# Optimization experiments

Measured on AMD Instinct MI355X. Metric: run time of the kernel, lower is better.

## Reference

```python
import jax, jax.numpy as jnp
import numpy as np

EMB = 1024
HEADS = 16
DEPTH = EMB // HEADS
B, S = 8, 1024


def setup_inputs() -> dict:
    key = jax.random.key(0)
    ks = jax.random.split(key, 12)
    sc = 0.02
    return {
        "q": jax.random.normal(ks[0], (B, S, EMB), jnp.float32),
        "k": jax.random.normal(ks[1], (B, S, EMB), jnp.float32),
        "v": jax.random.normal(ks[2], (B, S, EMB), jnp.float32),
        # per-head Dense weights stacked: [H, EMB, DEPTH], biases [H, DEPTH]
        "Wq": jax.random.normal(ks[3], (HEADS, EMB, DEPTH), jnp.float32) * sc,
        "bq": jnp.zeros((HEADS, DEPTH), jnp.float32),
        "Wk": jax.random.normal(ks[4], (HEADS, EMB, DEPTH), jnp.float32) * sc,
        "bk": jnp.zeros((HEADS, DEPTH), jnp.float32),
        "Wv": jax.random.normal(ks[5], (HEADS, EMB, DEPTH), jnp.float32) * sc,
        "bv": jnp.zeros((HEADS, DEPTH), jnp.float32),
        # output Dense: [EMB, EMB], bias [EMB]
        "Wo": jax.random.normal(ks[6], (EMB, EMB), jnp.float32) * sc,
        "bo": jnp.zeros((EMB,), jnp.float32),
    }


def reference(q, k, v, Wq, bq, Wk, bk, Wv, bv, Wo, bo):
    # Per-head Dense projections, batched over heads via einsum.
    # qh: [B, H, S, DEPTH]
    qh = jnp.einsum("bsd,hde->bhse", q, Wq) + bq[None, :, None, :]
    kh = jnp.einsum("bsd,hde->bhse", k, Wk) + bk[None, :, None, :]
    vh = jnp.einsum("bsd,hde->bhse", v, Wv) + bv[None, :, None, :]
    # Scaled dot-product attention per head: logits [B, H, Sq, Sk]
    scale = 1.0 / jnp.sqrt(jnp.asarray(DEPTH, jnp.float32))
    logits = jnp.einsum("bhqe,bhke->bhqk", qh, kh) * scale
    attn = jax.nn.softmax(logits, axis=-1)
    ctx = jnp.einsum("bhqk,bhke->bhqe", attn, vh)  # [B, H, S, DEPTH]
    # concat heads along last axis (head order preserved)
    ctx = jnp.transpose(ctx, (0, 2, 1, 3)).reshape(B, S, EMB)
    return ctx @ Wo + bo
```

## Files before the change

### kernel.cpp

```cpp
#include <hip/hip_runtime.h>
#include <hip/hip_bf16.h>
#include <stdint.h>

typedef __bf16 bf16;
typedef __attribute__((ext_vector_type(8))) __bf16 bf16x8;
typedef __attribute__((ext_vector_type(4))) float f32x4;

#define GLD(g, l) __builtin_amdgcn_global_load_lds( \
    (const __attribute__((address_space(1))) void*)(g), \
    (__attribute__((address_space(3))) void*)(l), 16, 0, 0)

__device__ __forceinline__ f32x4 mfma16(bf16x8 a, bf16x8 b, f32x4 c) {
  return __builtin_amdgcn_mfma_f32_16x16x32_bf16(a, b, c, 0, 0, 0);
}

__global__ __launch_bounds__(256) void cast_k(const float* __restrict__ s,
                                              bf16* __restrict__ d)
{
  const size_t i = ((size_t)blockIdx.x * 256 + threadIdx.x) * 8;
  float4 a = *(const float4*)(s + i);
  float4 b = *(const float4*)(s + i + 4);
  bf16x8 p;
  p[0] = (bf16)a.x; p[1] = (bf16)a.y; p[2] = (bf16)a.z; p[3] = (bf16)a.w;
  p[4] = (bf16)b.x; p[5] = (bf16)b.y; p[6] = (bf16)b.z; p[7] = (bf16)b.w;
  *(bf16x8*)(d + i) = p;
}

template <typename ST>
__global__ void transpose_k(const ST* __restrict__ src, bf16* __restrict__ dst,
                            int sld, int dld, int sdiv, int sA, int sB, int dA, int dB)
{
  __shared__ bf16 t[32][33];
  const int z = blockIdx.z;
  const ST* s = src + (size_t)(z / sdiv) * sA + (size_t)(z % sdiv) * sB;
  bf16* d = dst + (size_t)(z / sdiv) * dA + (size_t)(z % sdiv) * dB;
  const int c0 = blockIdx.x * 32, r0 = blockIdx.y * 32;
  const int tx = threadIdx.x, ty = threadIdx.y;
#pragma unroll
  for (int i = 0; i < 32; i += 8)
    t[ty + i][tx] = (bf16)(float)s[(r0 + ty + i) * sld + c0 + tx];
  __syncthreads();
#pragma unroll
  for (int i = 0; i < 32; i += 8)
    d[(c0 + ty + i) * dld + r0 + tx] = t[tx][ty + i];
}

__global__ __launch_bounds__(256) void gemm_bt(
    const bf16* __restrict__ A, const bf16* __restrict__ Bt,
    const float* __restrict__ bias, bf16* __restrict__ C,
    int M, int N, int K, float cmul)
{
  __shared__ bf16 sA[128 * 32];
  __shared__ bf16 sB[128 * 32];
  const int tid = threadIdx.x;
  const int wave = tid >> 6, lane = tid & 63;
  const int lr = lane & 15, kq = (lane >> 4) * 8;
  const int m0 = blockIdx.y * 128, n0 = blockIdx.x * 128;
  const int wr = (wave >> 1) * 64, wc = (wave & 1) * 64;

  f32x4 acc[4][4];
#pragma unroll
  for (int i = 0; i < 4; i++)
#pragma unroll
    for (int j = 0; j < 4; j++)
#pragma unroll
      for (int e = 0; e < 4; e++) acc[i][j][e] = 0.f;

  const int sRow = tid >> 2;
  const int sKo = (tid & 3) * 8;
  const bf16* aPtr = A + (size_t)(m0 + sRow) * K + sKo;
  const bf16* bPtr = Bt + (size_t)(n0 + sRow) * K + sKo;
  bf16* sAd = sA + tid * 8;
  bf16* sBd = sB + tid * 8;

  for (int k0 = 0; k0 < K; k0 += 32) {
    GLD(aPtr + k0,           sAd);
    GLD(aPtr + 64 * K + k0,  sAd + 2048);
    GLD(bPtr + k0,           sBd);
    GLD(bPtr + 64 * K + k0,  sBd + 2048);
    __syncthreads();
    bf16x8 af[4], bfr[4];
#pragma unroll
    for (int i = 0; i < 4; i++)
      af[i] = *(const bf16x8*)(sA + (wr + i * 16 + lr) * 32 + kq);
#pragma unroll
    for (int i = 0; i < 4; i++)
      bfr[i] = *(const bf16x8*)(sB + (wc + i * 16 + lr) * 32 + kq);
#pragma unroll
    for (int im = 0; im < 4; im++)
#pragma unroll
      for (int in = 0; in < 4; in++)
        acc[im][in] = mfma16(af[im], bfr[in], acc[im][in]);
    __syncthreads();
  }

  const int qd = (lane >> 4) * 4;
  float bv[4];
#pragma unroll
  for (int in = 0; in < 4; in++) bv[in] = bias[n0 + wc + in * 16 + lr];
#pragma unroll
  for (int im = 0; im < 4; im++) {
    const int row = m0 + wr + im * 16 + qd;
#pragma unroll
    for (int in = 0; in < 4; in++) {
      const int col = n0 + wc + in * 16 + lr;
#pragma unroll
      for (int i = 0; i < 4; i++)
        C[(size_t)(row + i) * N + col] = (bf16)((acc[im][in][i] + bv[in]) * cmul);
    }
  }
}

__global__ __launch_bounds__(256) void gemm_a16_c32(
    const bf16* __restrict__ A, const bf16* __restrict__ Bt,
    const float* __restrict__ bias, float* __restrict__ C,
    int M, int N, int K)
{
  __shared__ bf16 sA[128 * 32];
  __shared__ bf16 sB[128 * 32];
  const int tid = threadIdx.x;
  const int wave = tid >> 6, lane = tid & 63;
  const int lr = lane & 15, kq = (lane >> 4) * 8;
  const int m0 = blockIdx.y * 128, n0 = blockIdx.x * 128;
  const int wr = (wave >> 1) * 64, wc = (wave & 1) * 64;

  f32x4 acc[4][4];
#pragma unroll
  for (int i = 0; i < 4; i++)
#pragma unroll
    for (int j = 0; j < 4; j++)
#pragma unroll
      for (int e = 0; e < 4; e++) acc[i][j][e] = 0.f;

  const int sRow = tid >> 2;
  const int sKo = (tid & 3) * 8;
  const bf16* aPtr = A + (size_t)(m0 + sRow) * K + sKo;
  const bf16* bPtr = Bt + (size_t)(n0 + sRow) * K + sKo;
  bf16* sAd = sA + tid * 8;
  bf16* sBd = sB + tid * 8;

  for (int k0 = 0; k0 < K; k0 += 32) {
    GLD(aPtr + k0,           sAd);
    GLD(aPtr + 64 * K + k0,  sAd + 2048);
    GLD(bPtr + k0,           sBd);
    GLD(bPtr + 64 * K + k0,  sBd + 2048);
    __syncthreads();
    bf16x8 af[4], bfr[4];
#pragma unroll
    for (int i = 0; i < 4; i++)
      af[i] = *(const bf16x8*)(sA + (wr + i * 16 + lr) * 32 + kq);
#pragma unroll
    for (int i = 0; i < 4; i++)
      bfr[i] = *(const bf16x8*)(sB + (wc + i * 16 + lr) * 32 + kq);
#pragma unroll
    for (int im = 0; im < 4; im++)
#pragma unroll
      for (int in = 0; in < 4; in++)
        acc[im][in] = mfma16(af[im], bfr[in], acc[im][in]);
    __syncthreads();
  }

  const int qd = (lane >> 4) * 4;
  float bv[4];
#pragma unroll
  for (int in = 0; in < 4; in++) bv[in] = bias[n0 + wc + in * 16 + lr];
#pragma unroll
  for (int im = 0; im < 4; im++) {
    const int row = m0 + wr + im * 16 + qd;
#pragma unroll
    for (int in = 0; in < 4; in++) {
      const int col = n0 + wc + in * 16 + lr;
#pragma unroll
      for (int i = 0; i < 4; i++)
        C[(size_t)(row + i) * N + col] = acc[im][in][i] + bv[in];
    }
  }
}

__global__ __launch_bounds__(256) void attn_k(
    const bf16* __restrict__ Q, const bf16* __restrict__ Kh,
    const bf16* __restrict__ Vt, bf16* __restrict__ O)
{
  __shared__ bf16 sK[64 * 72];
  __shared__ bf16 sV[64 * 72];
  __shared__ bf16 sP[128 * 72];
  const int h = blockIdx.x, b = blockIdx.y, q0 = blockIdx.z * 128;
  const int tid = threadIdx.x, wave = tid >> 6, lane = tid & 63;
  const int lr = lane & 15, quad = lane >> 4, kq = quad * 8;
  const int wq = wave * 32;

  const bf16* Qb = Q + (size_t)(b * 1024 + q0) * 1024 + h * 64;
  const bf16* Kb = Kh + (size_t)(b * 1024) * 1024 + h * 64;
  const bf16* Vb = Vt + (size_t)(b * 16 + h) * 65536;

  bf16x8 qf[2][2];
#pragma unroll
  for (int rg = 0; rg < 2; rg++)
#pragma unroll
    for (int ks = 0; ks < 2; ks++)
      qf[rg][ks] = *(const bf16x8*)(Qb + (wq + rg * 16 + lr) * 1024 + ks * 32 + kq);

  f32x4 o[2][4];
  float rsum[2][4];
#pragma unroll
  for (int rg = 0; rg < 2; rg++) {
#pragma unroll
    for (int et = 0; et < 4; et++)
#pragma unroll
      for (int e = 0; e < 4; e++) o[rg][et][e] = 0.f;
#pragma unroll
    for (int i = 0; i < 4; i++) rsum[rg][i] = 0.f;
  }

  const int r = tid >> 3;
  const int c = (tid & 7) * 8;

  for (int kv0 = 0; kv0 < 1024; kv0 += 64) {
    bf16x8 k1 = *(const bf16x8*)(Kb + (size_t)(kv0 + r) * 1024 + c);
    bf16x8 k2 = *(const bf16x8*)(Kb + (size_t)(kv0 + 32 + r) * 1024 + c);
    bf16x8 v1 = *(const bf16x8*)(Vb + (size_t)r * 1024 + kv0 + c);
    bf16x8 v2 = *(const bf16x8*)(Vb + (size_t)(32 + r) * 1024 + kv0 + c);
    __syncthreads();
    *(bf16x8*)(sK + r * 72 + c) = k1;
    *(bf16x8*)(sK + (32 + r) * 72 + c) = k2;
    *(bf16x8*)(sV + r * 72 + c) = v1;
    *(bf16x8*)(sV + (32 + r) * 72 + c) = v2;
    __syncthreads();

    f32x4 sc[2][4];
#pragma unroll
    for (int nt = 0; nt < 4; nt++) {
      bf16x8 kf0 = *(const bf16x8*)(sK + (nt * 16 + lr) * 72 + kq);
      bf16x8 kf1 = *(const bf16x8*)(sK + (nt * 16 + lr) * 72 + 32 + kq);
#pragma unroll
      for (int rg = 0; rg < 2; rg++) {
        f32x4 z;
#pragma unroll
        for (int e = 0; e < 4; e++) z[e] = 0.f;
        z = mfma16(qf[rg][0], kf0, z);
        z = mfma16(qf[rg][1], kf1, z);
        sc[rg][nt] = z;
      }
    }

#pragma unroll
    for (int rg = 0; rg < 2; rg++)
#pragma unroll
      for (int i = 0; i < 4; i++) {
        float p0 = exp2f(sc[rg][0][i]);
        float p1 = exp2f(sc[rg][1][i]);
        float p2 = exp2f(sc[rg][2][i]);
        float p3 = exp2f(sc[rg][3][i]);
        rsum[rg][i] += (p0 + p1) + (p2 + p3);
        const int prow = (wq + rg * 16 + quad * 4 + i) * 72;
        sP[prow + 0 * 16 + lr] = (bf16)p0;
        sP[prow + 1 * 16 + lr] = (bf16)p1;
        sP[prow + 2 * 16 + lr] = (bf16)p2;
        sP[prow + 3 * 16 + lr] = (bf16)p3;
      }
    __syncthreads();

#pragma unroll
    for (int et = 0; et < 4; et++) {
      bf16x8 vf0 = *(const bf16x8*)(sV + (et * 16 + lr) * 72 + kq);
      bf16x8 vf1 = *(const bf16x8*)(sV + (et * 16 + lr) * 72 + 32 + kq);
#pragma unroll
      for (int rg = 0; rg < 2; rg++) {
        bf16x8 pa = *(const bf16x8*)(sP + (wq + rg * 16 + lr) * 72 + kq);
        bf16x8 pb = *(const bf16x8*)(sP + (wq + rg * 16 + lr) * 72 + 32 + kq);
        o[rg][et] = mfma16(pa, vf0, o[rg][et]);
        o[rg][et] = mfma16(pb, vf1, o[rg][et]);
      }
    }
  }

#pragma unroll
  for (int rg = 0; rg < 2; rg++)
#pragma unroll
    for (int i = 0; i < 4; i++) {
      float rs = rsum[rg][i];
#pragma unroll
      for (int off = 1; off < 16; off <<= 1)
        rs += __shfl_xor(rs, off, 64);
      rsum[rg][i] = 1.f / rs;
    }

  bf16* Ob = O + (size_t)(b * 1024 + q0) * 1024 + h * 64;
#pragma unroll
  for (int rg = 0; rg < 2; rg++)
#pragma unroll
    for (int i = 0; i < 4; i++) {
      const int row = wq + rg * 16 + quad * 4 + i;
#pragma unroll
      for (int et = 0; et < 4; et++)
        Ob[row * 1024 + et * 16 + lr] = (bf16)(o[rg][et][i] * rsum[rg][i]);
    }
}

extern "C" void kernel_launch(void* const* d_in, const int* in_sizes, int n_in,
                              void* d_out, int out_size, void* d_ws, size_t ws_size,
                              hipStream_t stream)
{
  const float* q  = (const float*)d_in[0];
  const float* k  = (const float*)d_in[1];
  const float* v  = (const float*)d_in[2];
  const float* Wq = (const float*)d_in[3];
  const float* bq = (const float*)d_in[4];
  const float* Wk = (const float*)d_in[5];
  const float* bk = (const float*)d_in[6];
  const float* Wv = (const float*)d_in[7];
  const float* bv = (const float*)d_in[8];
  const float* Wo = (const float*)d_in[9];
  const float* bo = (const float*)d_in[10];
  float* out = (float*)d_out;
  bf16* ws = (bf16*)d_ws;

  const int MB = 1 << 20;
  bf16* WqT = ws;
  bf16* WkT = ws + 1 * MB;
  bf16* WvT = ws + 2 * MB;
  bf16* WoT = ws + 3 * MB;
  bf16* qh  = ws + 4 * MB;
  bf16* kh  = ws + 12 * MB;
  bf16* vh  = ws + 20 * MB;
  bf16* qc  = (bf16*)d_out;
  bf16* vt  = (bf16*)d_out + 8 * MB;
  bf16* ctx = vh;

  const float cscale = 0.1803368801111601f;

  dim3 tb(32, 8);
  transpose_k<float><<<dim3(2, 32, 16), tb, 0, stream>>>(Wq, WqT, 64, 1024, 16, 0, 65536, 0, 65536);
  transpose_k<float><<<dim3(2, 32, 16), tb, 0, stream>>>(Wk, WkT, 64, 1024, 16, 0, 65536, 0, 65536);
  transpose_k<float><<<dim3(2, 32, 16), tb, 0, stream>>>(Wv, WvT, 64, 1024, 16, 0, 65536, 0, 65536);
  transpose_k<float><<<dim3(32, 32, 1), tb, 0, stream>>>(Wo, WoT, 1024, 1024, 1, 0, 0, 0, 0);

  cast_k<<<4096, 256, 0, stream>>>(q, qc);
  gemm_bt<<<dim3(8, 64), 256, 0, stream>>>(qc, WqT, bq, qh, 8192, 1024, 1024, cscale);
  cast_k<<<4096, 256, 0, stream>>>(k, qc);
  gemm_bt<<<dim3(8, 64), 256, 0, stream>>>(qc, WkT, bk, kh, 8192, 1024, 1024, 1.0f);
  cast_k<<<4096, 256, 0, stream>>>(v, qc);
  gemm_bt<<<dim3(8, 64), 256, 0, stream>>>(qc, WvT, bv, vh, 8192, 1024, 1024, 1.0f);

  transpose_k<bf16><<<dim3(2, 32, 128), tb, 0, stream>>>(vh, vt, 1024, 1024, 16,
                                                         1048576, 64, 1048576, 65536);

  attn_k<<<dim3(16, 8, 8), 256, 0, stream>>>(qh, kh, vt, ctx);

  gemm_a16_c32<<<dim3(8, 64), 256, 0, stream>>>(ctx, WoT, bo, out, 8192, 1024, 1024);
}
```

Before: 375.8 us.

## Fuse fp32 cast into batched QKV projection GEMM with swizzled K=64 tiles

Removes the three separate fp32-to-bf16 cast kernels and merges the three Q/K/V projection GEMMs into one launch that reads fp32 activations directly, converting them in registers before storing to shared memory. Both GEMMs now use a K-step of 64 with XOR-swizzled LDS layouts to reduce bank conflicts and halve barrier count per K. This cuts the extra global round-trip for the bf16 copies and launch overhead, at the cost of more LDS per block and register-held fp32 loads in the projection kernel.

```diff
diff --git a/kernel.cpp b/kernel.cpp
--- a/kernel.cpp
+++ b/kernel.cpp
@@ -12,18 +12,6 @@
 
 __device__ __forceinline__ f32x4 mfma16(bf16x8 a, bf16x8 b, f32x4 c) {
   return __builtin_amdgcn_mfma_f32_16x16x32_bf16(a, b, c, 0, 0, 0);
-}
-
-__global__ __launch_bounds__(256) void cast_k(const float* __restrict__ s,
-                                              bf16* __restrict__ d)
-{
-  const size_t i = ((size_t)blockIdx.x * 256 + threadIdx.x) * 8;
-  float4 a = *(const float4*)(s + i);
-  float4 b = *(const float4*)(s + i + 4);
-  bf16x8 p;
-  p[0] = (bf16)a.x; p[1] = (bf16)a.y; p[2] = (bf16)a.z; p[3] = (bf16)a.w;
-  p[4] = (bf16)b.x; p[5] = (bf16)b.y; p[6] = (bf16)b.z; p[7] = (bf16)b.w;
-  *(bf16x8*)(d + i) = p;
 }
 
 template <typename ST>
@@ -45,16 +33,110 @@
     d[(c0 + ty + i) * dld + r0 + tx] = t[tx][ty + i];
 }
 
-__global__ __launch_bounds__(256) void gemm_bt(
-    const bf16* __restrict__ A, const bf16* __restrict__ Bt,
-    const float* __restrict__ bias, bf16* __restrict__ C,
-    int M, int N, int K, float cmul)
-{
-  __shared__ bf16 sA[128 * 32];
-  __shared__ bf16 sB[128 * 32];
+__global__ __launch_bounds__(256) void proj_qkv(
+    const float* __restrict__ Aq, const float* __restrict__ Ak,
+    const float* __restrict__ Av, const bf16* __restrict__ WT,
+    const float* __restrict__ bq, const float* __restrict__ bk,
+    const float* __restrict__ bv, bf16* __restrict__ Cb,
+    float cscale)
+{
+  __shared__ bf16 sA[128 * 72];
+  __shared__ bf16 sB[128 * 64];
   const int tid = threadIdx.x;
   const int wave = tid >> 6, lane = tid & 63;
-  const int lr = lane & 15, kq = (lane >> 4) * 8;
+  const int lr = lane & 15, quad = lane >> 4, kq = quad * 8;
+  const int n0 = blockIdx.x * 128;
+  const int mseg = blockIdx.y * 128;
+  const int seg = mseg >> 13;
+  const int m0 = mseg & 8191;
+  const int wr = (wave >> 1) * 64, wc = (wave & 1) * 64;
+
+  const float* A = (seg == 0) ? Aq : (seg == 1) ? Ak : Av;
+  const float* bias = (seg == 0) ? bq : (seg == 1) ? bk : bv;
+  const float cmul = (seg == 0) ? cscale : 1.0f;
+  const bf16* Bt = WT + (size_t)seg * (1 << 20);
+  bf16* C = Cb + (size_t)seg * (8192 * 1024);
+
+  f32x4 acc[4][4];
+#pragma unroll
+  for (int i = 0; i < 4; i++)
+#pragma unroll
+    for (int j = 0; j < 4; j++)
+#pragma unroll
+      for (int e = 0; e < 4; e++) acc[i][j][e] = 0.f;
+
+  const int ar = tid >> 1, ach = (tid & 1) * 32;
+  const float* aPtr = A + (size_t)(m0 + ar) * 1024 + ach;
+  const int brow = tid >> 3;
+  const int bc = ((tid & 7) ^ (brow & 7)) * 8;
+  const bf16* bPtr = Bt + (size_t)(n0 + brow) * 1024 + bc;
+  bf16* sBd = sB + tid * 8;
+
+  for (int k0 = 0; k0 < 1024; k0 += 64) {
+    GLD(bPtr + k0,             sBd);
+    GLD(bPtr + 32 * 1024 + k0, sBd + 2048);
+    GLD(bPtr + 64 * 1024 + k0, sBd + 4096);
+    GLD(bPtr + 96 * 1024 + k0, sBd + 6144);
+    float4 f[8];
+#pragma unroll
+    for (int j = 0; j < 8; j++) f[j] = *(const float4*)(aPtr + k0 + j * 4);
+    __syncthreads();
+#pragma unroll
+    for (int j = 0; j < 4; j++) {
+      bf16x8 p;
+      p[0] = (bf16)f[2*j].x; p[1] = (bf16)f[2*j].y;
+      p[2] = (bf16)f[2*j].z; p[3] = (bf16)f[2*j].w;
+      p[4] = (bf16)f[2*j+1].x; p[5] = (bf16)f[2*j+1].y;
+      p[6] = (bf16)f[2*j+1].z; p[7] = (bf16)f[2*j+1].w;
+      *(bf16x8*)(sA + ar * 72 + ach + j * 8) = p;
+    }
+    __syncthreads();
+#pragma unroll
+    for (int kk = 0; kk < 64; kk += 32) {
+      bf16x8 af[4], bfr[4];
+#pragma unroll
+      for (int i = 0; i < 4; i++)
+        af[i] = *(const bf16x8*)(sA + (wr + i * 16 + lr) * 72 + kk + kq);
+#pragma unroll
+      for (int i = 0; i < 4; i++) {
+        const int pos = (((kk >> 3) + quad) ^ (lr & 7)) * 8;
+        bfr[i] = *(const bf16x8*)(sB + (wc + i * 16 + lr) * 64 + pos);
+      }
+#pragma unroll
+      for (int im = 0; im < 4; im++)
+#pragma unroll
+        for (int in = 0; in < 4; in++)
+          acc[im][in] = mfma16(af[im], bfr[in], acc[im][in]);
+    }
+  }
+  __syncthreads();
+
+  const int qd = quad * 4;
+  float bv4[4];
+#pragma unroll
+  for (int in = 0; in < 4; in++) bv4[in] = bias[n0 + wc + in * 16 + lr];
+#pragma unroll
+  for (int im = 0; im < 4; im++) {
+    const int row = m0 + wr + im * 16 + qd;
+#pragma unroll
+    for (int in = 0; in < 4; in++) {
+      const int col = n0 + wc + in * 16 + lr;
+#pragma unroll
+      for (int i = 0; i < 4; i++)
+        C[(size_t)(row + i) * 1024 + col] = (bf16)((acc[im][in][i] + bv4[in]) * cmul);
+    }
+  }
+}
+
+__global__ __launch_bounds__(256) void gemm_a16_c32(
+    const bf16* __restrict__ A, const bf16* __restrict__ Bt,
+    const float* __restrict__ bias, float* __restrict__ C)
+{
+  __shared__ bf16 sA[128 * 64];
+  __shared__ bf16 sB[128 * 64];
+  const int tid = threadIdx.x;
+  const int wave = tid >> 6, lane = tid & 63;
+  const int lr = lane & 15, quad = lane >> 4, kq = quad * 8;
   const int m0 = blockIdx.y * 128, n0 = blockIdx.x * 128;
   const int wr = (wave >> 1) * 64, wc = (wave & 1) * 64;
 
@@ -66,38 +148,45 @@
 #pragma unroll
       for (int e = 0; e < 4; e++) acc[i][j][e] = 0.f;
 
-  const int sRow = tid >> 2;
-  const int sKo = (tid & 3) * 8;
-  const bf16* aPtr = A + (size_t)(m0 + sRow) * K + sKo;
-  const bf16* bPtr = Bt + (size_t)(n0 + sRow) * K + sKo;
+  const int srow = tid >> 3;
+  const int sc = ((tid & 7) ^ (srow & 7)) * 8;
+  const bf16* aPtr = A + (size_t)(m0 + srow) * 1024 + sc;
+  const bf16* bPtr = Bt + (size_t)(n0 + srow) * 1024 + sc;
   bf16* sAd = sA + tid * 8;
   bf16* sBd = sB + tid * 8;
 
-  for (int k0 = 0; k0 < K; k0 += 32) {
-    GLD(aPtr + k0,           sAd);
-    GLD(aPtr + 64 * K + k0,  sAd + 2048);
-    GLD(bPtr + k0,           sBd);
-    GLD(bPtr + 64 * K + k0,  sBd + 2048);
-    __syncthreads();
-    bf16x8 af[4], bfr[4];
-#pragma unroll
-    for (int i = 0; i < 4; i++)
-      af[i] = *(const bf16x8*)(sA + (wr + i * 16 + lr) * 32 + kq);
-#pragma unroll
-    for (int i = 0; i < 4; i++)
-      bfr[i] = *(const bf16x8*)(sB + (wc + i * 16 + lr) * 32 + kq);
-#pragma unroll
-    for (int im = 0; im < 4; im++)
-#pragma unroll
-      for (int in = 0; in < 4; in++)
-        acc[im][in] = mfma16(af[im], bfr[in], acc[im][in]);
-    __syncthreads();
-  }
-
-  const int qd = (lane >> 4) * 4;
-  float bv[4];
-#pragma unroll
-  for (int in = 0; in < 4; in++) bv[in] = bias[n0 + wc + in * 16 + lr];
+  for (int k0 = 0; k0 < 1024; k0 += 64) {
+    GLD(aPtr + k0,             sAd);
+    GLD(aPtr + 32 * 1024 + k0, sAd + 2048);
+    GLD(aPtr + 64 * 1024 + k0, sAd + 4096);
+    GLD(aPtr + 96 * 1024 + k0, sAd + 6144);
+    GLD(bPtr + k0,             sBd);
+    GLD(bPtr + 32 * 1024 + k0, sBd + 2048);
+    GLD(bPtr + 64 * 1024 + k0, sBd + 4096);
+    GLD(bPtr + 96 * 1024 + k0, sBd + 6144);
+    __syncthreads();
+#pragma unroll
+    for (int kk = 0; kk < 64; kk += 32) {
+      bf16x8 af[4], bfr[4];
+#pragma unroll
+      for (int i = 0; i < 4; i++) {
+        const int pos = (((kk >> 3) + quad) ^ (lr & 7)) * 8;
+        af[i]  = *(const bf16x8*)(sA + (wr + i * 16 + lr) * 64 + pos);
+        bfr[i] = *(const bf16x8*)(sB + (wc + i * 16 + lr) * 64 + pos);
+      }
+#pragma unroll
+      for (int im = 0; im < 4; im++)
+#pragma unroll
+        for (int in = 0; in < 4; in++)
+          acc[im][in] = mfma16(af[im], bfr[in], acc[im][in]);
+    }
+    __syncthreads();
+  }
+
+  const int qd = quad * 4;
+  float bv4[4];
+#pragma unroll
+  for (int in = 0; in < 4; in++) bv4[in] = bias[n0 + wc + in * 16 + lr];
 #pragma unroll
   for (int im = 0; im < 4; im++) {
     const int row = m0 + wr + im * 16 + qd;
@@ -106,73 +195,7 @@
       const int col = n0 + wc + in * 16 + lr;
 #pragma unroll
       for (int i = 0; i < 4; i++)
-        C[(size_t)(row + i) * N + col] = (bf16)((acc[im][in][i] + bv[in]) * cmul);
-    }
-  }
-}
-
-__global__ __launch_bounds__(256) void gemm_a16_c32(
-    const bf16* __restrict__ A, const bf16* __restrict__ Bt,
-    const float* __restrict__ bias, float* __restrict__ C,
-    int M, int N, int K)
-{
-  __shared__ bf16 sA[128 * 32];
-  __shared__ bf16 sB[128 * 32];
-  const int tid = threadIdx.x;
-  const int wave = tid >> 6, lane = tid & 63;
-  const int lr = lane & 15, kq = (lane >> 4) * 8;
-  const int m0 = blockIdx.y * 128, n0 = blockIdx.x * 128;
-  const int wr = (wave >> 1) * 64, wc = (wave & 1) * 64;
-
-  f32x4 acc[4][4];
-#pragma unroll
-  for (int i = 0; i < 4; i++)
-#pragma unroll
-    for (int j = 0; j < 4; j++)
-#pragma unroll
-      for (int e = 0; e < 4; e++) acc[i][j][e] = 0.f;
-
-  const int sRow = tid >> 2;
-  const int sKo = (tid & 3) * 8;
-  const bf16* aPtr = A + (size_t)(m0 + sRow) * K + sKo;
-  const bf16* bPtr = Bt + (size_t)(n0 + sRow) * K + sKo;
-  bf16* sAd = sA + tid * 8;
-  bf16* sBd = sB + tid * 8;
-
-  for (int k0 = 0; k0 < K; k0 += 32) {
-    GLD(aPtr + k0,           sAd);
-    GLD(aPtr + 64 * K + k0,  sAd + 2048);
-    GLD(bPtr + k0,           sBd);
-    GLD(bPtr + 64 * K + k0,  sBd + 2048);
-    __syncthreads();
-    bf16x8 af[4], bfr[4];
-#pragma unroll
-    for (int i = 0; i < 4; i++)
-      af[i] = *(const bf16x8*)(sA + (wr + i * 16 + lr) * 32 + kq);
-#pragma unroll
-    for (int i = 0; i < 4; i++)
-      bfr[i] = *(const bf16x8*)(sB + (wc + i * 16 + lr) * 32 + kq);
-#pragma unroll
-    for (int im = 0; im < 4; im++)
-#pragma unroll
-      for (int in = 0; in < 4; in++)
-        acc[im][in] = mfma16(af[im], bfr[in], acc[im][in]);
-    __syncthreads();
-  }
-
-  const int qd = (lane >> 4) * 4;
-  float bv[4];
-#pragma unroll
-  for (int in = 0; in < 4; in++) bv[in] = bias[n0 + wc + in * 16 + lr];
-#pragma unroll
-  for (int im = 0; im < 4; im++) {
-    const int row = m0 + wr + im * 16 + qd;
-#pragma unroll
-    for (int in = 0; in < 4; in++) {
-      const int col = n0 + wc + in * 16 + lr;
-#pragma unroll
-      for (int i = 0; i < 4; i++)
-        C[(size_t)(row + i) * N + col] = acc[im][in][i] + bv[in];
+        C[(size_t)(row + i) * 1024 + col] = acc[im][in][i] + bv4[in];
     }
   }
 }
@@ -316,36 +339,29 @@
   bf16* ws = (bf16*)d_ws;
 
   const int MB = 1 << 20;
-  bf16* WqT = ws;
-  bf16* WkT = ws + 1 * MB;
-  bf16* WvT = ws + 2 * MB;
+  bf16* WT  = ws;
   bf16* WoT = ws + 3 * MB;
-  bf16* qh  = ws + 4 * MB;
-  bf16* kh  = ws + 12 * MB;
-  bf16* vh  = ws + 20 * MB;
-  bf16* qc  = (bf16*)d_out;
-  bf16* vt  = (bf16*)d_out + 8 * MB;
+  bf16* qkv = ws + 4 * MB;
+  bf16* qh  = qkv;
+  bf16* kh  = qkv + 8 * MB;
+  bf16* vh  = qkv + 16 * MB;
+  bf16* vt  = (bf16*)d_out;
   bf16* ctx = vh;
 
   const float cscale = 0.1803368801111601f;
 
   dim3 tb(32, 8);
-  transpose_k<float><<<dim3(2, 32, 16), tb, 0, stream>>>(Wq, WqT, 64, 1024, 16, 0, 65536, 0, 65536);
-  transpose_k<float><<<dim3(2, 32, 16), tb, 0, stream>>>(Wk, WkT, 64, 1024, 16, 0, 65536, 0, 65536);
-  transpose_k<float><<<dim3(2, 32, 16), tb, 0, stream>>>(Wv, WvT, 64, 1024, 16, 0, 65536, 0, 65536);
+  transpose_k<float><<<dim3(2, 32, 16), tb, 0, stream>>>(Wq, WT,          64, 1024, 16, 0, 65536, 0, 65536);
+  transpose_k<float><<<dim3(2, 32, 16), tb, 0, stream>>>(Wk, WT + 1 * MB, 64, 1024, 16, 0, 65536, 0, 65536);
+  transpose_k<float><<<dim3(2, 32, 16), tb, 0, stream>>>(Wv, WT + 2 * MB, 64, 1024, 16, 0, 65536, 0, 65536);
   transpose_k<float><<<dim3(32, 32, 1), tb, 0, stream>>>(Wo, WoT, 1024, 1024, 1, 0, 0, 0, 0);
 
-  cast_k<<<4096, 256, 0, stream>>>(q, qc);
-  gemm_bt<<<dim3(8, 64), 256, 0, stream>>>(qc, WqT, bq, qh, 8192, 1024, 1024, cscale);
-  cast_k<<<4096, 256, 0, stream>>>(k, qc);
-  gemm_bt<<<dim3(8, 64), 256, 0, stream>>>(qc, WkT, bk, kh, 8192, 1024, 1024, 1.0f);
-  cast_k<<<4096, 256, 0, stream>>>(v, qc);
-  gemm_bt<<<dim3(8, 64), 256, 0, stream>>>(qc, WvT, bv, vh, 8192, 1024, 1024, 1.0f);
+  proj_qkv<<<dim3(8, 192), 256, 0, stream>>>(q, k, v, WT, bq, bk, bv, qkv, cscale);
 
   transpose_k<bf16><<<dim3(2, 32, 128), tb, 0, stream>>>(vh, vt, 1024, 1024, 16,
                                                          1048576, 64, 1048576, 65536);
 
   attn_k<<<dim3(16, 8, 8), 256, 0, stream>>>(qh, kh, vt, ctx);
 
-  gemm_a16_c32<<<dim3(8, 64), 256, 0, stream>>>(ctx, WoT, bo, out, 8192, 1024, 1024);
-}
+  gemm_a16_c32<<<dim3(8, 64), 256, 0, stream>>>(ctx, WoT, bo, out);
+}
```

Result: slower. 396.6 us (+5.5%).
